# Kernel optimization log

Hardware: AMD Instinct MI355X
Metric: run time of the kernel (lower is better)

## Reference

```python
import jax, jax.numpy as jnp
import numpy as np

B, D, UNITS, C = 16384, 1024, 1500, 2000  # batch, embed_dim, leaves, total classes
N_NORM = 2.0
EPS = 1e-6


def setup_inputs() -> dict:
    key = jax.random.key(0)
    k_in, k_w, k_r = jax.random.split(key, 3)
    inputs = jax.random.normal(k_in, (B, D), dtype=jnp.float32)
    # glorot init for linear (embedding_dim, units)
    scale = jnp.sqrt(6.0 / (D + UNITS)).astype(jnp.float32)
    linear = jax.random.uniform(k_w, (D, UNITS), dtype=jnp.float32, minval=-scale, maxval=scale)
    bias = jnp.zeros((UNITS,), dtype=jnp.float32)
    # R_t: (n_classes, units) 0/1 ancestor mask. Leaf classes (first UNITS rows)
    # map to themselves (identity); internal classes get random leaf descendants.
    leaf_rows = jnp.eye(UNITS, dtype=jnp.float32)
    anc_rows = (jax.random.uniform(k_r, (C - UNITS, UNITS)) < 0.05).astype(jnp.float32)
    R_t = jnp.concatenate([leaf_rows, anc_rows], axis=0)
    return {"inputs": inputs, "linear": linear, "bias": bias, "R_t": R_t}


def reference(inputs, linear, bias, R_t):
    # sigmoid linear layer: (B, UNITS)
    out = jax.nn.sigmoid(inputs @ linear + bias)
    # n>1 branch: n_norm(out[:, None, :] * R_t).
    # Because R_t is a 0/1 mask, (out_j * R_t[c, j])**n == R_t[c, j] * out_j**n,
    # so the broadcast-multiply + pow + sum fuses exactly into a masked matmul.
    s = (out ** N_NORM) @ R_t.T               # (B, C) = sum over leaves
    s = jnp.clip(s, EPS, 1.0 - EPS)
    return s ** (1.0 / N_NORM)
```

## Files before the change

### kernel.cpp

```cpp
#include <hip/hip_runtime.h>
#include <stdint.h>

#define BROWS 16384
#define DDIM 1024
#define UNITSN 1500
#define UNITSP 1536
#define CCLS 2000
#define NINT 500
#define NINTP 512
#define EPSV 1e-6f
#define LEAF_LO 1e-3f
#define LEAF_HI 0.9999995f

typedef __bf16 bf16x8 __attribute__((ext_vector_type(8)));
typedef float f32x4 __attribute__((ext_vector_type(4)));
typedef unsigned short u16x4v __attribute__((ext_vector_type(4)));

__device__ __forceinline__ unsigned short f2bf(float f) {
  union { float f; uint32_t u; } x; x.f = f;
  uint32_t r = x.u + 0x7fffu + ((x.u >> 16) & 1u);
  return (unsigned short)(r >> 16);
}

__device__ __forceinline__ float fast_rcp(float x) {
  float r; asm("v_rcp_f32 %0, %1" : "=v"(r) : "v"(x)); return r;
}
__device__ __forceinline__ float fast_sqrt(float x) {
  float r; asm("v_sqrt_f32 %0, %1" : "=v"(r) : "v"(x)); return r;
}

__device__ __forceinline__ void gload_lds16(const void* g, void* l) {
  __builtin_amdgcn_global_load_lds(
      reinterpret_cast<const __attribute__((address_space(1))) void*>(
          reinterpret_cast<uintptr_t>(g)),
      reinterpret_cast<__attribute__((address_space(3))) void*>(
          (uint32_t)reinterpret_cast<uintptr_t>(l)),
      16, 0, 0);
}

#define VMW(n) asm volatile("s_waitcnt vmcnt(" #n ")" ::: "memory")
#define LGKM0() asm volatile("s_waitcnt lgkmcnt(0)" ::: "memory")
#define SBAR() __builtin_amdgcn_s_barrier()
#define SCHED0() __builtin_amdgcn_sched_barrier(0)
#define MFMA __builtin_amdgcn_mfma_f32_16x16x32_bf16

__global__ __launch_bounds__(256) void k_prep(
    const float* __restrict__ inputs, const float* __restrict__ lin,
    const float* __restrict__ R, unsigned short* __restrict__ Ab,
    unsigned short* __restrict__ wt, unsigned short* __restrict__ Rb) {
  const int b = blockIdx.x, t = threadIdx.x;

  if (b < 1536) {
    __shared__ float tle[32][33];
    const int nb = (b % 48) * 32;
    const int kb = (b / 48) * 32;
    const int tx = t & 31, ty = t >> 5;
#pragma unroll
    for (int s = 0; s < 32; s += 8) {
      int k = kb + ty + s, n = nb + tx;
      tle[ty + s][tx] = (n < UNITSN) ? lin[k * UNITSN + n] : 0.f;
    }
    __syncthreads();
#pragma unroll
    for (int s = 0; s < 32; s += 8) {
      int n = nb + ty + s, k = kb + tx;
      wt[n * DDIM + k] = f2bf(tle[tx][ty + s]);
    }
  }

  const int gtid = b * 256 + t;
  const float4* in4 = (const float4*)inputs;
  for (int i = gtid; i < (BROWS * DDIM) / 4; i += 2048 * 256) {
    float4 v = in4[i];
    u16x4v o;
    o.x = f2bf(v.x); o.y = f2bf(v.y); o.z = f2bf(v.z); o.w = f2bf(v.w);
    *reinterpret_cast<u16x4v*>(Ab + i * 4) = o;
  }

  for (int i = gtid; i < NINTP * UNITSP; i += 2048 * 256) {
    int r = i / UNITSP;
    int u = i - r * UNITSP;
    float v = (r < NINT && u < UNITSN) ? R[(size_t)(UNITSN + r) * UNITSN + u] : 0.f;
    Rb[i] = f2bf(v);
  }
}

__global__ __launch_bounds__(256, 3) void k_gemm1c(
    const unsigned short* __restrict__ A,
    const unsigned short* __restrict__ Bt,
    const float* __restrict__ bias,
    unsigned short* __restrict__ o2,
    float* __restrict__ outf) {
  constexpr int K = DDIM;
  constexpr int NKT = K / 64;
  constexpr int NBX = 12;
  __shared__ char smem[32768];

  const int nwg = (int)gridDim.x;
  const int qx = nwg >> 3;
  const int bid = (int)blockIdx.x;
  const int wg = (bid & 7) * qx + (bid >> 3);
  const int bx = wg % NBX, by = wg / NBX;
  const int brow = by << 7, bcol = bx << 7;

  const int tid = (int)threadIdx.x;
  const int lane = tid & 63;
  const int w = tid >> 6;
  const int wr = w >> 1, wc = w & 1;

  const unsigned short* gA =
      A + (size_t)(brow + (tid >> 3)) * K + (((tid & 7) ^ ((tid >> 3) & 7)) << 3);
  const unsigned short* gB =
      Bt + (size_t)(bcol + (tid >> 3)) * K + (((tid & 7) ^ ((tid >> 3) & 7)) << 3);
  const int sW = w << 10;

  const int s0 = (((lane >> 4) ^ (lane & 7)) << 4);
  const int aOff = (((wr << 6) + (lane & 15)) << 7) + s0;
  const int bOff = 16384 + (((wc << 6) + (lane & 15)) << 7) + s0;

#define STG8(t) do { \
    gload_lds16(gA + (size_t)(t) * 64,                    smem + 0     + sW); \
    gload_lds16(gA + (size_t)32 * K + (size_t)(t) * 64,   smem + 4096  + sW); \
    gload_lds16(gA + (size_t)64 * K + (size_t)(t) * 64,   smem + 8192  + sW); \
    gload_lds16(gA + (size_t)96 * K + (size_t)(t) * 64,   smem + 12288 + sW); \
    gload_lds16(gB + (size_t)(t) * 64,                    smem + 16384 + sW); \
    gload_lds16(gB + (size_t)32 * K + (size_t)(t) * 64,   smem + 20480 + sW); \
    gload_lds16(gB + (size_t)64 * K + (size_t)(t) * 64,   smem + 24576 + sW); \
    gload_lds16(gB + (size_t)96 * K + (size_t)(t) * 64,   smem + 28672 + sW); \
  } while (0)
#define LDA1(i, ks) (*reinterpret_cast<const bf16x8*>(smem + (aOff ^ ((ks) * 64)) + (i) * 2048))
#define LDB1(j, ks) (*reinterpret_cast<const bf16x8*>(smem + (bOff ^ ((ks) * 64)) + (j) * 2048))

  f32x4 acc[4][4] = {};

  for (int t = 0; t < NKT; ++t) {
    STG8(t);
    __syncthreads();
    bf16x8 a0[4], a1[4], b0[4], b1[4];
#pragma unroll
    for (int i = 0; i < 4; ++i) { a0[i] = LDA1(i, 0); a1[i] = LDA1(i, 1); }
#pragma unroll
    for (int j = 0; j < 4; ++j) { b0[j] = LDB1(j, 0); b1[j] = LDB1(j, 1); }
#pragma unroll
    for (int i = 0; i < 4; ++i)
#pragma unroll
      for (int j = 0; j < 4; ++j) {
        acc[i][j] = MFMA(a0[i], b0[j], acc[i][j], 0, 0, 0);
        acc[i][j] = MFMA(a1[i], b1[j], acc[i][j], 0, 0, 0);
      }
    __syncthreads();
  }
#undef STG8
#undef LDA1
#undef LDB1

#pragma unroll
  for (int i = 0; i < 4; ++i) {
    const int row0 = brow + (wr << 6) + i * 16 + ((lane >> 4) << 2);
#pragma unroll
    for (int j = 0; j < 4; ++j) {
      const int col = bcol + (wc << 6) + j * 16 + (lane & 15);
      const bool live = (col < UNITSN);
      float bz = live ? bias[col] : 0.f;
#pragma unroll
      for (int r = 0; r < 4; ++r) {
        float z = acc[i][j][r] + bz;
        float sg = fast_rcp(1.f + __expf(-z));
        float s2 = sg * sg;
        o2[(size_t)(row0 + r) * UNITSP + col] = f2bf(live ? s2 : 0.f);
        if (live) {
          outf[(size_t)(row0 + r) * CCLS + col] = fminf(fmaxf(sg, LEAF_LO), LEAF_HI);
        }
      }
    }
  }
}

template <int NBX, int K>
__global__ __launch_bounds__(512, 4) void k_g128i(
    const unsigned short* __restrict__ A,
    const unsigned short* __restrict__ Bt,
    float* __restrict__ outf) {
  constexpr int NKT = K / 64;
  constexpr int BUFS = 32768;
  __shared__ char smem[2 * BUFS];

  const int nwg = (int)gridDim.x;
  const int qx = nwg >> 3;
  const int bid = (int)blockIdx.x;
  const int wg = (bid & 7) * qx + (bid >> 3);
  const int bx = wg % NBX, by = wg / NBX;
  const int brow = by << 7, bcol = bx << 7;

  const int tid = (int)threadIdx.x;
  const int lane = tid & 63;
  const int w = tid >> 6;
  const int wr = w >> 2, wc = w & 3;

  const unsigned short* gA =
      A + (size_t)(brow + (w << 3) + (lane >> 3)) * K + (((lane & 7) ^ (lane >> 3)) << 3);
  const unsigned short* gB =
      Bt + (size_t)(bcol + (w << 3) + (lane >> 3)) * K + (((lane & 7) ^ (lane >> 3)) << 3);
  const int sW = w << 10;

  const int s0 = (((lane >> 4) ^ (lane & 7)) << 4);
  const int aRB = (((wr << 6) + (lane & 15)) << 7);
  const int bRB = 16384 + (((wc << 5) + (lane & 15)) << 7);

#define STA2(b, u, gt) gload_lds16(gA + (size_t)((u) * 64) * K + (size_t)(gt) * 64, \
                                   smem + ((b) * BUFS + (u) * 8192) + sW)
#define STB2(b, u, gt) gload_lds16(gB + (size_t)((u) * 64) * K + (size_t)(gt) * 64, \
                                   smem + ((b) * BUFS + 16384 + (u) * 8192) + sW)
#define LDA2(b, i, ks) (*reinterpret_cast<const bf16x8*>( \
    smem + (b) * BUFS + aRB + (i) * 2048 + (s0 ^ ((ks) * 64))))
#define LDB2(b, j, ks) (*reinterpret_cast<const bf16x8*>( \
    smem + (b) * BUFS + bRB + (j) * 2048 + (s0 ^ ((ks) * 64))))

  f32x4 acc[4][2] = {};
  bf16x8 Bf0[2], Bf1[2];

  STB2(0, 0, 0); STB2(0, 1, 0);
  STA2(0, 0, 0); STA2(0, 1, 0);
  STB2(1, 0, 1); STB2(1, 1, 1);
  VMW(2);
  SBAR(); SCHED0();

  for (int it = 0; it < NKT / 2; ++it) {
    const int tb = 2 * it + 1, t2 = 2 * it + 2, t3 = 2 * it + 3;
    {
      bf16x8 a00 = LDA2(0, 0, 0), a01 = LDA2(0, 0, 1);
      bf16x8 a10 = LDA2(0, 1, 0), a11 = LDA2(0, 1, 1);
#pragma unroll
      for (int j = 0; j < 2; ++j) { Bf0[j] = LDB2(0, j, 0); Bf1[j] = LDB2(0, j, 1); }
      STA2(1, 0, tb); STA2(1, 1, tb);
      SBAR(); LGKM0(); SCHED0();
      __builtin_amdgcn_s_setprio(1);
#pragma unroll
      for (int j = 0; j < 2; ++j) { acc[0][j] = MFMA(a00, Bf0[j], acc[0][j], 0, 0, 0);
                                    acc[1][j] = MFMA(a10, Bf0[j], acc[1][j], 0, 0, 0); }
#pragma unroll
      for (int j = 0; j < 2; ++j) { acc[0][j] = MFMA(a01, Bf1[j], acc[0][j], 0, 0, 0);
                                    acc[1][j] = MFMA(a11, Bf1[j], acc[1][j], 0, 0, 0); }
      __builtin_amdgcn_s_setprio(0);
      SBAR(); SCHED0();
    }
    {
      bf16x8 a00 = LDA2(0, 2, 0), a01 = LDA2(0, 2, 1);
      bf16x8 a10 = LDA2(0, 3, 0), a11 = LDA2(0, 3, 1);
      if (t2 < NKT) { STB2(0, 0, t2); STB2(0, 1, t2); }
      SBAR(); LGKM0(); SCHED0();
      __builtin_amdgcn_s_setprio(1);
#pragma unroll
      for (int j = 0; j < 2; ++j) { acc[2][j] = MFMA(a00, Bf0[j], acc[2][j], 0, 0, 0);
                                    acc[3][j] = MFMA(a10, Bf0[j], acc[3][j], 0, 0, 0); }
#pragma unroll
      for (int j = 0; j < 2; ++j) { acc[2][j] = MFMA(a01, Bf1[j], acc[2][j], 0, 0, 0);
                                    acc[3][j] = MFMA(a11, Bf1[j], acc[3][j], 0, 0, 0); }
      __builtin_amdgcn_s_setprio(0);
      if (t2 < NKT) { VMW(2); } else { VMW(0); }
      SBAR(); SCHED0();
    }
    {
      bf16x8 a00 = LDA2(1, 0, 0), a01 = LDA2(1, 0, 1);
      bf16x8 a10 = LDA2(1, 1, 0), a11 = LDA2(1, 1, 1);
#pragma unroll
      for (int j = 0; j < 2; ++j) { Bf0[j] = LDB2(1, j, 0); Bf1[j] = LDB2(1, j, 1); }
      if (t2 < NKT) { STA2(0, 0, t2); STA2(0, 1, t2); }
      SBAR(); LGKM0(); SCHED0();
      __builtin_amdgcn_s_setprio(1);
#pragma unroll
      for (int j = 0; j < 2; ++j) { acc[0][j] = MFMA(a00, Bf0[j], acc[0][j], 0, 0, 0);
                                    acc[1][j] = MFMA(a10, Bf0[j], acc[1][j], 0, 0, 0); }
#pragma unroll
      for (int j = 0; j < 2; ++j) { acc[0][j] = MFMA(a01, Bf1[j], acc[0][j], 0, 0, 0);
                                    acc[1][j] = MFMA(a11, Bf1[j], acc[1][j], 0, 0, 0); }
      __builtin_amdgcn_s_setprio(0);
      SBAR(); SCHED0();
    }
    {
      bf16x8 a00 = LDA2(1, 2, 0), a01 = LDA2(1, 2, 1);
      bf16x8 a10 = LDA2(1, 3, 0), a11 = LDA2(1, 3, 1);
      if (t3 < NKT) { STB2(1, 0, t3); STB2(1, 1, t3); }
      SBAR(); LGKM0(); SCHED0();
      __builtin_amdgcn_s_setprio(1);
#pragma unroll
      for (int j = 0; j < 2; ++j) { acc[2][j] = MFMA(a00, Bf0[j], acc[2][j], 0, 0, 0);
                                    acc[3][j] = MFMA(a10, Bf0[j], acc[3][j], 0, 0, 0); }
#pragma unroll
      for (int j = 0; j < 2; ++j) { acc[2][j] = MFMA(a01, Bf1[j], acc[2][j], 0, 0, 0);
                                    acc[3][j] = MFMA(a11, Bf1[j], acc[3][j], 0, 0, 0); }
      __builtin_amdgcn_s_setprio(0);
      if (t3 < NKT) { VMW(2); }
      SBAR(); SCHED0();
    }
  }

#pragma unroll
  for (int i = 0; i < 4; ++i) {
    const int row0 = brow + (wr << 6) + i * 16 + ((lane >> 4) << 2);
#pragma unroll
    for (int j = 0; j < 2; ++j) {
      const int col = bcol + (wc << 5) + j * 16 + (lane & 15);
      if (col < NINT) {
#pragma unroll
        for (int r = 0; r < 4; ++r) {
          float s = acc[i][j][r];
          s = fminf(fmaxf(s, EPSV), 1.f - EPSV);
          outf[(size_t)(row0 + r) * CCLS + UNITSN + col] = fast_sqrt(s);
        }
      }
    }
  }
#undef STA2
#undef STB2
#undef LDA2
#undef LDB2
}


extern "C" void kernel_launch(void* const* d_in, const int* in_sizes, int n_in,
                              void* d_out, int out_size, void* d_ws, size_t ws_size,
                              hipStream_t stream) {
  const float* inputs = (const float*)d_in[0];
  const float* linear = (const float*)d_in[1];
  const float* bias   = (const float*)d_in[2];
  const float* R_t    = (const float*)d_in[3];
  float* out = (float*)d_out;

  char* ws = (char*)d_ws;
  unsigned short* Ab  = (unsigned short*)(ws);
  unsigned short* Wt  = (unsigned short*)(ws + 33554432);
  unsigned short* RbI = (unsigned short*)(ws + 36700160);
  unsigned short* O2  = (unsigned short*)(ws + 38273024);

  k_prep<<<2048, 256, 0, stream>>>(inputs, linear, R_t, Ab, Wt, RbI);

  k_gemm1c<<<1536, 256, 0, stream>>>(Ab, Wt, bias, O2, out);
  k_g128i<4, UNITSP><<<512, 512, 0, stream>>>(O2, RbI, out);
}
```

Before: 122.2 us.

## Fuse fp32-to-bf16 input conversion into GEMM1 with register-staged double buffering

Removes the separate pass that converted the 64MB fp32 input to a bf16 workspace. GEMM1 now loads fp32 A tiles straight into registers, converts them, and writes bf16 into swizzled LDS. It double-buffers both operands (64KB LDS) so the next tile's loads overlap the current MFMAs. This saves a full write and reread of the bf16 copy, but each GEMM block rereads fp32 A per column tile (12x) and occupancy drops from 3 to 2 blocks per CU.

```diff
diff --git a/kernel.cpp b/kernel.cpp
--- a/kernel.cpp
+++ b/kernel.cpp
@@ -44,13 +44,12 @@
 #define SCHED0() __builtin_amdgcn_sched_barrier(0)
 #define MFMA __builtin_amdgcn_mfma_f32_16x16x32_bf16
 
-__global__ __launch_bounds__(256) void k_prep(
-    const float* __restrict__ inputs, const float* __restrict__ lin,
-    const float* __restrict__ R, unsigned short* __restrict__ Ab,
+__global__ __launch_bounds__(256) void k_prep2(
+    const float* __restrict__ lin, const float* __restrict__ R,
     unsigned short* __restrict__ wt, unsigned short* __restrict__ Rb) {
   const int b = blockIdx.x, t = threadIdx.x;
 
-  if (b < 1536) {
+  {
     __shared__ float tle[32][33];
     const int nb = (b % 48) * 32;
     const int kb = (b / 48) * 32;
@@ -69,15 +68,7 @@
   }
 
   const int gtid = b * 256 + t;
-  const float4* in4 = (const float4*)inputs;
-  for (int i = gtid; i < (BROWS * DDIM) / 4; i += 2048 * 256) {
-    float4 v = in4[i];
-    u16x4v o;
-    o.x = f2bf(v.x); o.y = f2bf(v.y); o.z = f2bf(v.z); o.w = f2bf(v.w);
-    *reinterpret_cast<u16x4v*>(Ab + i * 4) = o;
-  }
-
-  for (int i = gtid; i < NINTP * UNITSP; i += 2048 * 256) {
+  for (int i = gtid; i < NINTP * UNITSP; i += 1536 * 256) {
     int r = i / UNITSP;
     int u = i - r * UNITSP;
     float v = (r < NINT && u < UNITSN) ? R[(size_t)(UNITSN + r) * UNITSN + u] : 0.f;
@@ -85,16 +76,16 @@
   }
 }
 
-__global__ __launch_bounds__(256, 3) void k_gemm1c(
-    const unsigned short* __restrict__ A,
+__global__ __launch_bounds__(256, 2) void k_gemm1d(
+    const float* __restrict__ Af,
     const unsigned short* __restrict__ Bt,
     const float* __restrict__ bias,
     unsigned short* __restrict__ o2,
     float* __restrict__ outf) {
   constexpr int K = DDIM;
-  constexpr int NKT = K / 64;
+  constexpr int NKT = 16;
   constexpr int NBX = 12;
-  __shared__ char smem[32768];
+  __shared__ char smem[65536];
 
   const int nwg = (int)gridDim.x;
   const int qx = nwg >> 3;
@@ -108,39 +99,62 @@
   const int w = tid >> 6;
   const int wr = w >> 1, wc = w & 1;
 
-  const unsigned short* gA =
-      A + (size_t)(brow + (tid >> 3)) * K + (((tid & 7) ^ ((tid >> 3) & 7)) << 3);
+  const int ar = tid >> 4;
+  const int ac = tid & 15;
+  const float4* gAf =
+      reinterpret_cast<const float4*>(Af) + (size_t)(brow + ar) * (K / 4) + ac;
+  const int aw = ar * 128 + ((((ac >> 1) ^ (ar & 7)) << 4)) + ((ac & 1) << 3);
+
   const unsigned short* gB =
       Bt + (size_t)(bcol + (tid >> 3)) * K + (((tid & 7) ^ ((tid >> 3) & 7)) << 3);
   const int sW = w << 10;
 
   const int s0 = (((lane >> 4) ^ (lane & 7)) << 4);
   const int aOff = (((wr << 6) + (lane & 15)) << 7) + s0;
-  const int bOff = 16384 + (((wc << 6) + (lane & 15)) << 7) + s0;
-
-#define STG8(t) do { \
-    gload_lds16(gA + (size_t)(t) * 64,                    smem + 0     + sW); \
-    gload_lds16(gA + (size_t)32 * K + (size_t)(t) * 64,   smem + 4096  + sW); \
-    gload_lds16(gA + (size_t)64 * K + (size_t)(t) * 64,   smem + 8192  + sW); \
-    gload_lds16(gA + (size_t)96 * K + (size_t)(t) * 64,   smem + 12288 + sW); \
-    gload_lds16(gB + (size_t)(t) * 64,                    smem + 16384 + sW); \
-    gload_lds16(gB + (size_t)32 * K + (size_t)(t) * 64,   smem + 20480 + sW); \
-    gload_lds16(gB + (size_t)64 * K + (size_t)(t) * 64,   smem + 24576 + sW); \
-    gload_lds16(gB + (size_t)96 * K + (size_t)(t) * 64,   smem + 28672 + sW); \
+  const int bOff = 32768 + (((wc << 6) + (lane & 15)) << 7) + s0;
+
+#define GLB(p, t) do { \
+    gload_lds16(gB + (size_t)(t) * 64,                  smem + 32768 + (p) * 16384 + 0     + sW); \
+    gload_lds16(gB + (size_t)32 * K + (size_t)(t) * 64, smem + 32768 + (p) * 16384 + 4096  + sW); \
+    gload_lds16(gB + (size_t)64 * K + (size_t)(t) * 64, smem + 32768 + (p) * 16384 + 8192  + sW); \
+    gload_lds16(gB + (size_t)96 * K + (size_t)(t) * 64, smem + 32768 + (p) * 16384 + 12288 + sW); \
   } while (0)
-#define LDA1(i, ks) (*reinterpret_cast<const bf16x8*>(smem + (aOff ^ ((ks) * 64)) + (i) * 2048))
-#define LDB1(j, ks) (*reinterpret_cast<const bf16x8*>(smem + (bOff ^ ((ks) * 64)) + (j) * 2048))
+#define AWRITE(p) do { \
+    _Pragma("unroll") \
+    for (int j = 0; j < 8; ++j) { \
+      u16x4v v_; \
+      v_.x = f2bf(aR[j].x); v_.y = f2bf(aR[j].y); \
+      v_.z = f2bf(aR[j].z); v_.w = f2bf(aR[j].w); \
+      *reinterpret_cast<u16x4v*>(smem + (p) * 16384 + j * 2048 + aw) = v_; \
+    } \
+  } while (0)
+#define LDA1(p, i, ks) (*reinterpret_cast<const bf16x8*>( \
+    smem + (p) * 16384 + ((aOff + (i) * 2048) ^ ((ks) * 64))))
+#define LDB1(p, j, ks) (*reinterpret_cast<const bf16x8*>( \
+    smem + (p) * 16384 + ((bOff + (j) * 2048) ^ ((ks) * 64))))
 
   f32x4 acc[4][4] = {};
+  float4 aR[8];
+
+#pragma unroll
+  for (int j = 0; j < 8; ++j) aR[j] = gAf[(size_t)j * 16 * (K / 4)];
+  GLB(0, 0);
+  AWRITE(0);
+  __syncthreads();
 
   for (int t = 0; t < NKT; ++t) {
-    STG8(t);
-    __syncthreads();
+    const int p = t & 1;
+    if (t < NKT - 1) {
+#pragma unroll
+      for (int j = 0; j < 8; ++j)
+        aR[j] = gAf[(size_t)j * 16 * (K / 4) + (size_t)(t + 1) * 16];
+      GLB(p ^ 1, t + 1);
+    }
     bf16x8 a0[4], a1[4], b0[4], b1[4];
 #pragma unroll
-    for (int i = 0; i < 4; ++i) { a0[i] = LDA1(i, 0); a1[i] = LDA1(i, 1); }
-#pragma unroll
-    for (int j = 0; j < 4; ++j) { b0[j] = LDB1(j, 0); b1[j] = LDB1(j, 1); }
+    for (int i = 0; i < 4; ++i) { a0[i] = LDA1(p, i, 0); a1[i] = LDA1(p, i, 1); }
+#pragma unroll
+    for (int j = 0; j < 4; ++j) { b0[j] = LDB1(p, j, 0); b1[j] = LDB1(p, j, 1); }
 #pragma unroll
     for (int i = 0; i < 4; ++i)
 #pragma unroll
@@ -148,9 +162,13 @@
         acc[i][j] = MFMA(a0[i], b0[j], acc[i][j], 0, 0, 0);
         acc[i][j] = MFMA(a1[i], b1[j], acc[i][j], 0, 0, 0);
       }
+    if (t < NKT - 1) {
+      AWRITE(p ^ 1);
+    }
     __syncthreads();
   }
-#undef STG8
+#undef GLB
+#undef AWRITE
 #undef LDA1
 #undef LDB1
 
@@ -328,13 +346,12 @@
   float* out = (float*)d_out;
 
   char* ws = (char*)d_ws;
-  unsigned short* Ab  = (unsigned short*)(ws);
-  unsigned short* Wt  = (unsigned short*)(ws + 33554432);
-  unsigned short* RbI = (unsigned short*)(ws + 36700160);
-  unsigned short* O2  = (unsigned short*)(ws + 38273024);
-
-  k_prep<<<2048, 256, 0, stream>>>(inputs, linear, R_t, Ab, Wt, RbI);
-
-  k_gemm1c<<<1536, 256, 0, stream>>>(Ab, Wt, bias, O2, out);
+  unsigned short* Wt  = (unsigned short*)(ws);
+  unsigned short* RbI = (unsigned short*)(ws + 3145728);
+  unsigned short* O2  = (unsigned short*)(ws + 4718592);
+
+  k_prep2<<<1536, 256, 0, stream>>>(linear, R_t, Wt, RbI);
+
+  k_gemm1d<<<1536, 256, 0, stream>>>(inputs, Wt, bias, O2, out);
   k_g128i<4, UNITSP><<<512, 512, 0, stream>>>(O2, RbI, out);
 }
```

Measured after the change: 160.7 us. +31.5%, slower.
